# Optimization experiments

Measured on AMD Instinct MI355X. Metric: run time of the kernel, lower is better.

## Reference

```python
import jax, jax.numpy as jnp
import numpy as np

EPS = 1e-5

def _layernorm(x, gamma, beta):
    # normalize over last (channel) axis, per point
    mu = jnp.mean(x, axis=-1, keepdims=True)
    var = jnp.mean(jnp.square(x - mu), axis=-1, keepdims=True)
    return (x - mu) * jax.lax.rsqrt(var + EPS) * gamma + beta

def setup_inputs() -> dict:
    key = jax.random.key(0)
    ks = jax.random.split(key, 12)
    B, N, C, F = 32, 4096, 3, 1024
    points = jax.random.normal(ks[0], (B, N, C), dtype=jnp.float32)
    mask = jax.random.randint(ks[1], (B, 1, N), 0, 2, dtype=jnp.int32)
    s = 0.05
    return {
        "points": points,
        "mask": mask,
        "w1": jax.random.normal(ks[2], (128, C), dtype=jnp.float32) * s,      # conv1 (no bias)
        "g1": jnp.ones((128,), jnp.float32),                                   # norm1 gamma
        "be1": jnp.zeros((128,), jnp.float32),                                 # norm1 beta
        "w2": jax.random.normal(ks[3], (256, 128), dtype=jnp.float32) * s,     # conv2
        "b2": jax.random.normal(ks[4], (256,), dtype=jnp.float32) * s,
        "w3": jax.random.normal(ks[5], (512, 512), dtype=jnp.float32) * s,     # conv3 (no bias)
        "g2": jnp.ones((512,), jnp.float32),                                   # norm2 gamma
        "be2": jnp.zeros((512,), jnp.float32),                                 # norm2 beta
        "w4": jax.random.normal(ks[6], (F, 512), dtype=jnp.float32) * s,       # conv4
        "b4": jax.random.normal(ks[7], (F,), dtype=jnp.float32) * s,
    }

def reference(points, mask, w1, g1, be1, w2, b2, w3, g2, be2, w4, b4):
    # points: [B, N, C]; mask: [B, 1, N]
    vis = (mask[:, 0, :] != 0).astype(points.dtype)[..., None]  # [B, N, 1]
    # conv1 (1x1, no bias) as point-wise matmul
    h0 = jnp.einsum('bnc,kc->bnk', points, w1)                  # [B, N, 128]
    # masked LayerNorm: LN is per-point over channels, so compute densely and zero invisible points
    h1 = _layernorm(h0, g1, be1) * vis
    h2 = jax.nn.relu(h1)
    h3 = jnp.einsum('bnk,ok->bno', h2, w2) + b2                 # [B, N, 256]
    gmax = jnp.max(h3, axis=1, keepdims=True)                   # [B, 1, 256]
    dist = jnp.concatenate([jnp.broadcast_to(gmax, h3.shape), h3], axis=-1)  # [B, N, 512]
    h4 = jnp.einsum('bno,po->bnp', dist, w3)                    # [B, N, 512]
    h5 = _layernorm(h4, g2, be2) * vis
    h6 = jax.nn.relu(h5)
    h7 = jnp.einsum('bnp,fp->bnf', h6, w4) + b4                 # [B, N, F]
    return jnp.max(h7, axis=1)                                  # [B, F]
```

## Files before the change

### kernel.cpp

```cpp
#include <hip/hip_runtime.h>
#include <stdint.h>

#define LN_EPS 1e-5f

static __device__ __forceinline__ unsigned short f2bf_bits(float f) {
  union { float f; unsigned u; } v; v.f = f;
  unsigned r = v.u + 0x7FFFu + ((v.u >> 16) & 1u);
  return (unsigned short)(r >> 16);
}
static __device__ __forceinline__ float bf2f(unsigned short h) {
  union { unsigned u; float f; } v; v.u = ((unsigned)h) << 16;
  return v.f;
}

typedef __bf16 bf16x8 __attribute__((ext_vector_type(8)));
typedef float floatx4 __attribute__((ext_vector_type(4)));

typedef __attribute__((address_space(1))) unsigned int* gas_ptr;
typedef __attribute__((address_space(3))) unsigned int* las_ptr;
static __device__ __forceinline__ void async_cp16(const void* g, void* l) {
  __builtin_amdgcn_global_load_lds((gas_ptr)g, (las_ptr)l, 16, 0, 0);
}

__global__ __launch_bounds__(256) void perm_kernel(
    const int* __restrict__ mask, int* __restrict__ newrow, int* __restrict__ cnt) {
  const int b = blockIdx.x, t = threadIdx.x;
  const int base = b * 4096 + t * 16;
  int v[16]; int s = 0;
#pragma unroll
  for (int i = 0; i < 16; ++i) { v[i] = (mask[base + i] != 0); s += v[i]; }
  const int lane = t & 63, wv = t >> 6;
  int scan = s;
  for (int o = 1; o < 64; o <<= 1) { int x = __shfl_up(scan, o); if (lane >= o) scan += x; }
  __shared__ int wsum[4], woff[4], stotal;
  if (lane == 63) wsum[wv] = scan;
  __syncthreads();
  if (t == 0) { int a = 0; for (int k = 0; k < 4; ++k) { woff[k] = a; a += wsum[k]; } stotal = a; cnt[b] = a; }
  __syncthreads();
  const int excl = scan - s + woff[wv];
  const int total = stotal;
  int run = 0;
#pragma unroll
  for (int i = 0; i < 16; ++i) {
    const int pos = t * 16 + i;
    const int visBefore = excl + run;
    newrow[b * 4096 + pos] = v[i] ? visBefore : total + (pos - visBefore);
    run += v[i];
  }
}

__global__ __launch_bounds__(256) void conv1_ln_kernel(
    const float* __restrict__ points,
    const float* __restrict__ w1, const float* __restrict__ g1,
    const float* __restrict__ be1, unsigned short* __restrict__ h2,
    const int* __restrict__ newrow, const int* __restrict__ cnt,
    const float* __restrict__ w2, const float* __restrict__ b2,
    const float* __restrict__ w3, const float* __restrict__ w4,
    unsigned short* __restrict__ w2b, unsigned short* __restrict__ w4b,
    unsigned short* __restrict__ w23b, float* __restrict__ vecb) {
  if (blockIdx.x >= 32768) {
    const int bb = blockIdx.x - 32768;
    if (bb < 2176) {
      int idx = bb * 256 + threadIdx.x;
      if (idx < 32768) w2b[idx] = f2bf_bits(w2[idx]);
      else w4b[idx - 32768] = f2bf_bits(w4[idx - 32768]);
    } else {
      const int tid = threadIdx.x;
      const int p = (bb - 2176) * 2 + (tid >> 7);
      const int c = tid & 127;
      const float* w3r = w3 + (size_t)p * 512 + 256;
      float s = 0.f;
      for (int k = 0; k < 256; ++k) s += w3r[k] * w2[k * 128 + c];
      w23b[p * 128 + c] = f2bf_bits(s);
      if (c == 0) {
        float vb = 0.f;
        for (int k = 0; k < 256; ++k) vb += w3r[k] * b2[k];
        vecb[p] = vb;
      }
    }
    return;
  }
  const int lane = threadIdx.x & 63;
  const int wv = threadIdx.x >> 6;
  const size_t p = (size_t)blockIdx.x * 4 + wv;
  const int dest = newrow[p];
  const int cntb = cnt[p >> 12];
  const int ceilv = (cntb + 127) & ~127;
  if (dest >= ceilv) return;
  const bool vis = (dest < cntb);
  const float x0 = points[p * 3 + 0];
  const float x1 = points[p * 3 + 1];
  const float x2 = points[p * 3 + 2];
  const int c0 = lane * 2, c1 = c0 + 1;
  float h00 = w1[c0 * 3] * x0 + w1[c0 * 3 + 1] * x1 + w1[c0 * 3 + 2] * x2;
  float h01 = w1[c1 * 3] * x0 + w1[c1 * 3 + 1] * x1 + w1[c1 * 3 + 2] * x2;
  float s = h00 + h01;
  for (int o = 32; o; o >>= 1) s += __shfl_xor(s, o);
  const float mu = s * (1.f / 128.f);
  const float d0 = h00 - mu, d1 = h01 - mu;
  float q = d0 * d0 + d1 * d1;
  for (int o = 32; o; o >>= 1) q += __shfl_xor(q, o);
  const float rs = rsqrtf(q * (1.f / 128.f) + LN_EPS);
  const float y0 = vis ? fmaxf(d0 * rs * g1[c0] + be1[c0], 0.f) : 0.f;
  const float y1 = vis ? fmaxf(d1 * rs * g1[c1] + be1[c1], 0.f) : 0.f;
  union { unsigned u; unsigned short s2[2]; } pk;
  pk.s2[0] = f2bf_bits(y0);
  pk.s2[1] = f2bf_bits(y1);
  const size_t prow = (p & ~(size_t)4095) + (size_t)dest;
  ((unsigned*)h2)[prow * 64 + lane] = pk.u;
}

template <int EPI, int NCT>
__global__ __launch_bounds__(256) void gemm_bt(
    const unsigned short* __restrict__ A, const unsigned short* __restrict__ Bw,
    void* __restrict__ outp, float* __restrict__ outp2,
    const float* __restrict__ extra, const int* __restrict__ cnt,
    int M, int N, int K) {
  __shared__ __align__(16) char smA[2][128 * 64];
  __shared__ __align__(16) char smB[2][128 * 64];
  __shared__ float lmax[2][128];

  const int tid = threadIdx.x;
  const int lane = tid & 63;
  const int w = tid >> 6;
  const int wm = w >> 1, wn = w & 1;

  const int gid = blockIdx.x;
  const int xcd = gid & 7;
  const int slot = gid >> 3;
  const int rowsPerXcd = (M >> 7) >> 3;
  const int rowTile = xcd * rowsPerXcd + slot / NCT;
  const int colTile = slot % NCT;
  const size_t rowBase = (size_t)rowTile * 128;
  const int colBase = colTile * 128;

  const int cntb = cnt[rowBase >> 12];
  const int rb = (int)(rowBase & 4095);
  if (rb >= cntb) {
    if (EPI == 0) return;
    if (EPI == 2) {
      if (tid < 128) outp2[(size_t)rowTile * N + colBase + tid] = 0.f;
      return;
    }
    if (EPI == 4) {
      if (tid < 128) outp2[(size_t)rowTile * N + colBase + tid] = extra[colBase + tid];
      return;
    }
  }

  floatx4 acc[4][4];
  const floatx4 zero = {0.f, 0.f, 0.f, 0.f};
#pragma unroll
  for (int i = 0; i < 4; ++i)
#pragma unroll
    for (int j = 0; j < 4; ++j) acc[i][j] = zero;

  const int rSub = lane >> 2;
  const int cb16 = (lane & 3) * 16;
  const size_t Kb = (size_t)K * 2;
  const char* gA = (const char*)A + (rowBase + (size_t)(w * 32 + rSub)) * Kb + cb16;
  const char* gB = (const char*)Bw + ((size_t)colBase + (size_t)(w * 32 + rSub)) * Kb + cb16;
  char* lA0 = smA[0] + w * 2048;
  char* lA1 = smA[1] + w * 2048;
  char* lB0 = smB[0] + w * 2048;
  char* lB1 = smB[1] + w * 2048;
  const size_t skip16 = 16 * Kb;

  const int fm = lane & 15, fq = lane >> 4;
  const int fOff = fm * 64 + fq * 16;
  const char* pa0 = smA[0] + wm * 64 * 64 + fOff;
  const char* pa1 = smA[1] + wm * 64 * 64 + fOff;
  const char* pb0 = smB[0] + wn * 64 * 64 + fOff;
  const char* pb1 = smB[1] + wn * 64 * 64 + fOff;

  for (int k0 = 0; k0 < K; k0 += 64) {
    async_cp16(gA, lA0);
    async_cp16(gA + skip16, lA0 + 1024);
    async_cp16(gA + 64, lA1);
    async_cp16(gA + 64 + skip16, lA1 + 1024);
    async_cp16(gB, lB0);
    async_cp16(gB + skip16, lB0 + 1024);
    async_cp16(gB + 64, lB1);
    async_cp16(gB + 64 + skip16, lB1 + 1024);
    gA += 128; gB += 128;
    __syncthreads();
    bf16x8 af0[4], bg0[4], af1[4], bg1[4];
#pragma unroll
    for (int i = 0; i < 4; ++i) af0[i] = *(const bf16x8*)(pa0 + i * 16 * 64);
#pragma unroll
    for (int j = 0; j < 4; ++j) bg0[j] = *(const bf16x8*)(pb0 + j * 16 * 64);
#pragma unroll
    for (int i = 0; i < 4; ++i)
#pragma unroll
      for (int j = 0; j < 4; ++j)
        acc[i][j] = __builtin_amdgcn_mfma_f32_16x16x32_bf16(af0[i], bg0[j], acc[i][j], 0, 0, 0);
#pragma unroll
    for (int i = 0; i < 4; ++i) af1[i] = *(const bf16x8*)(pa1 + i * 16 * 64);
#pragma unroll
    for (int j = 0; j < 4; ++j) bg1[j] = *(const bf16x8*)(pb1 + j * 16 * 64);
#pragma unroll
    for (int i = 0; i < 4; ++i)
#pragma unroll
      for (int j = 0; j < 4; ++j)
        acc[i][j] = __builtin_amdgcn_mfma_f32_16x16x32_bf16(af1[i], bg1[j], acc[i][j], 0, 0, 0);
    __syncthreads();
  }

  float m4[4] = {-1e30f, -1e30f, -1e30f, -1e30f};

  if (EPI == 0) {
    unsigned short* O = (unsigned short*)outp;
#pragma unroll
    for (int j = 0; j < 4; ++j) {
      const int col = colBase + wn * 64 + j * 16 + fm;
      const float ex = extra[col];
#pragma unroll
      for (int i = 0; i < 4; ++i) {
        const size_t row0 = rowBase + wm * 64 + i * 16 + fq * 4;
#pragma unroll
        for (int r = 0; r < 4; ++r) {
          O[(row0 + r) * (size_t)N + col] = f2bf_bits(acc[i][j][r] + ex);
        }
      }
    }
  } else if (EPI == 2) {
#pragma unroll
    for (int j = 0; j < 4; ++j)
#pragma unroll
      for (int i = 0; i < 4; ++i)
#pragma unroll
        for (int r = 0; r < 4; ++r) m4[j] = fmaxf(m4[j], acc[i][j][r]);
  } else {
#pragma unroll
    for (int j = 0; j < 4; ++j) {
      const float ex = extra[colBase + wn * 64 + j * 16 + fm];
#pragma unroll
      for (int i = 0; i < 4; ++i)
#pragma unroll
        for (int r = 0; r < 4; ++r) m4[j] = fmaxf(m4[j], acc[i][j][r] + ex);
    }
  }

  if (EPI == 2 || EPI == 4) {
#pragma unroll
    for (int j = 0; j < 4; ++j) {
      m4[j] = fmaxf(m4[j], __shfl_xor(m4[j], 16));
      m4[j] = fmaxf(m4[j], __shfl_xor(m4[j], 32));
    }
    const float sel = (fq == 0) ? m4[0] : (fq == 1) ? m4[1] : (fq == 2) ? m4[2] : m4[3];
    lmax[wm][wn * 64 + fq * 16 + fm] = sel;
    __syncthreads();
    if (tid < 128) {
      const float v = fmaxf(lmax[0][tid], lmax[1][tid]);
      outp2[(size_t)rowTile * N + colBase + tid] = v;
    }
  }
}

__global__ __launch_bounds__(256) void gmax_cvec_kernel(
    const float* __restrict__ pg, const float* __restrict__ w3,
    float* __restrict__ cvec) {
  __shared__ float gm[256];
  const int b = blockIdx.x, t = threadIdx.x;
  float m = -1e30f;
  for (int s = 0; s < 32; ++s) m = fmaxf(m, pg[((size_t)b * 32 + s) * 256 + t]);
  gm[t] = m;
  __syncthreads();
#pragma unroll
  for (int half = 0; half < 2; ++half) {
    const int p = half * 256 + t;
    const float* wr = w3 + (size_t)p * 512;
    float s = 0.f;
    for (int c = 0; c < 256; ++c) s += wr[c] * gm[c];
    cvec[b * 512 + p] = s;
  }
}

__global__ __launch_bounds__(256) void ln2_kernel(
    unsigned short* __restrict__ h46, const int* __restrict__ cnt,
    const float* __restrict__ cvec,
    const float* __restrict__ g2, const float* __restrict__ be2) {
  const int lane = threadIdx.x & 63;
  const int wv = threadIdx.x >> 6;
  const size_t p = (size_t)blockIdx.x * 4 + wv;
  const int cb = cnt[p >> 12];
  const int pin = (int)(p & 4095);
  const int ceilv = (cb + 127) & ~127;
  if (pin >= ceilv) return;
  unsigned short* row = h46 + p * 512;
  const int c0 = lane * 8;
  if (pin >= cb) {
    const uint4 z = {0, 0, 0, 0};
    *(uint4*)(row + c0) = z;
    return;
  }
  const int b = (int)(p >> 12);
  union { uint4 v; unsigned short s[8]; } in;
  in.v = *(const uint4*)(row + c0);
  float cv[8];
  *(float4*)(cv) = *(const float4*)(cvec + b * 512 + c0);
  *(float4*)(cv + 4) = *(const float4*)(cvec + b * 512 + c0 + 4);
  float f[8];
  float s = 0.f;
#pragma unroll
  for (int k = 0; k < 8; ++k) { f[k] = bf2f(in.s[k]) + cv[k]; s += f[k]; }
  for (int o = 32; o; o >>= 1) s += __shfl_xor(s, o);
  const float mu = s * (1.f / 512.f);
  float q = 0.f;
#pragma unroll
  for (int k = 0; k < 8; ++k) { const float d = f[k] - mu; q += d * d; }
  for (int o = 32; o; o >>= 1) q += __shfl_xor(q, o);
  const float rs = rsqrtf(q * (1.f / 512.f) + LN_EPS);
  union { uint4 v; unsigned short s[8]; } outv;
#pragma unroll
  for (int k = 0; k < 8; ++k) {
    const float y = fmaxf((f[k] - mu) * rs * g2[c0 + k] + be2[c0 + k], 0.f);
    outv.s[k] = f2bf_bits(y);
  }
  *(uint4*)(row + c0) = outv.v;
}

__global__ __launch_bounds__(256) void final_kernel(
    const float* __restrict__ pmax, const float* __restrict__ b4,
    float* __restrict__ out) {
  const int idx = blockIdx.x * 256 + threadIdx.x;
  const int b = idx >> 10, f = idx & 1023;
  float m = -1e30f;
  for (int r = 0; r < 32; ++r) m = fmaxf(m, pmax[((size_t)(b * 32 + r)) * 1024 + f]);
  out[idx] = m + b4[f];
}

extern "C" void kernel_launch(void* const* d_in, const int* in_sizes, int n_in,
                              void* d_out, int out_size, void* d_ws, size_t ws_size,
                              hipStream_t stream) {
  const float* points = (const float*)d_in[0];
  const int* mask = (const int*)d_in[1];
  const float* w1 = (const float*)d_in[2];
  const float* g1 = (const float*)d_in[3];
  const float* be1 = (const float*)d_in[4];
  const float* w2 = (const float*)d_in[5];
  const float* b2 = (const float*)d_in[6];
  const float* w3 = (const float*)d_in[7];
  const float* g2 = (const float*)d_in[8];
  const float* be2 = (const float*)d_in[9];
  const float* w4 = (const float*)d_in[10];
  const float* b4 = (const float*)d_in[11];
  float* out = (float*)d_out;
  char* ws = (char*)d_ws;

  const size_t OFF_H46 = 0;
  const size_t OFF_H2 = 134217728;
  const size_t OFF_W2B = OFF_H2 + 33554432;
  const size_t OFF_W4B = OFF_W2B + 65536;
  const size_t OFF_W23B = OFF_W4B + 1048576;
  const size_t OFF_VECB = OFF_W23B + 131072;
  const size_t OFF_PG = OFF_VECB + 2048;
  const size_t OFF_CVEC = OFF_PG + 1048576;
  const size_t OFF_PMAX = OFF_CVEC + 65536;
  const size_t OFF_CNT = OFF_PMAX + 4194304;
  const size_t OFF_NEWROW = OFF_CNT + 4096;

  unsigned short* h2 = (unsigned short*)(ws + OFF_H2);
  unsigned short* h46 = (unsigned short*)(ws + OFF_H46);
  unsigned short* w2b = (unsigned short*)(ws + OFF_W2B);
  unsigned short* w4b = (unsigned short*)(ws + OFF_W4B);
  unsigned short* w23b = (unsigned short*)(ws + OFF_W23B);
  float* vecb = (float*)(ws + OFF_VECB);
  float* pg = (float*)(ws + OFF_PG);
  float* cvecp = (float*)(ws + OFF_CVEC);
  float* pmaxp = (float*)(ws + OFF_PMAX);
  int* cntp = (int*)(ws + OFF_CNT);
  int* newrow = (int*)(ws + OFF_NEWROW);

  perm_kernel<<<32, 256, 0, stream>>>(mask, newrow, cntp);
  conv1_ln_kernel<<<32768 + 2176 + 256, 256, 0, stream>>>(
      points, w1, g1, be1, h2, newrow, cntp, w2, b2, w3, w4, w2b, w4b, w23b, vecb);
  gemm_bt<4, 2><<<2048, 256, 0, stream>>>(h2, w2b, nullptr, pg, b2, cntp, 131072, 256, 128);
  gmax_cvec_kernel<<<32, 256, 0, stream>>>(pg, w3, cvecp);
  gemm_bt<0, 4><<<4096, 256, 0, stream>>>(h2, w23b, (void*)h46, nullptr, vecb, cntp, 131072, 512, 128);
  ln2_kernel<<<32768, 256, 0, stream>>>(h46, cntp, cvecp, g2, be2);
  gemm_bt<2, 8><<<8192, 256, 0, stream>>>(h46, w4b, nullptr, pmaxp, nullptr, cntp, 131072, 1024, 512);
  final_kernel<<<128, 256, 0, stream>>>(pmaxp, b4, out);
}
```

Before: 283.8 us.

## Fuse conv2 max-pool GEMM and conv3 local GEMM into one launch; parallelize cvec

Merges the two GEMMs that both read h2 (the conv2 row-max GEMM and the w23 local-term GEMM) into a single kernel with six column tiles per row tile. The first two tiles produce per-tile maxima and the rest write bf16 h46, so one launch replaces two and h2 tiles can be reused through cache. The gmax_cvec kernel is spread over 128 blocks using float4 loads and wave shuffles instead of 32 blocks of serial dot products. The old templated GEMM is specialised into a max-only variant for the final layer. Risks are divergent epilogues within one grid and extra register pressure.

```diff
diff --git a/kernel.cpp b/kernel.cpp
--- a/kernel.cpp
+++ b/kernel.cpp
@@ -110,11 +110,139 @@
   ((unsigned*)h2)[prow * 64 + lane] = pk.u;
 }
 
-template <int EPI, int NCT>
-__global__ __launch_bounds__(256) void gemm_bt(
+__global__ __launch_bounds__(256) void gemm23_fused(
+    const unsigned short* __restrict__ A,
+    const unsigned short* __restrict__ w2b, const unsigned short* __restrict__ w23b,
+    unsigned short* __restrict__ h46, float* __restrict__ pg,
+    const float* __restrict__ b2, const float* __restrict__ vecb,
+    const int* __restrict__ cnt, int M) {
+  __shared__ __align__(16) char smA[2][128 * 64];
+  __shared__ __align__(16) char smB[2][128 * 64];
+  __shared__ float lmax[2][128];
+
+  const int tid = threadIdx.x;
+  const int lane = tid & 63;
+  const int w = tid >> 6;
+  const int wm = w >> 1, wn = w & 1;
+
+  const int gid = blockIdx.x;
+  const int xcd = gid & 7;
+  const int slot = gid >> 3;
+  const int rowsPerXcd = (M >> 7) >> 3;
+  const int rowTile = xcd * rowsPerXcd + slot / 6;
+  const int colTile = slot % 6;
+  const bool isPG = (colTile < 2);
+  const int colBase = isPG ? colTile * 128 : (colTile - 2) * 128;
+  const size_t rowBase = (size_t)rowTile * 128;
+  const unsigned short* Bw = isPG ? w2b : w23b;
+
+  const int cntb = cnt[rowBase >> 12];
+  const int rb = (int)(rowBase & 4095);
+  if (rb >= cntb) {
+    if (isPG) {
+      if (tid < 128) pg[(size_t)rowTile * 256 + colBase + tid] = b2[colBase + tid];
+    }
+    return;
+  }
+
+  floatx4 acc[4][4];
+  const floatx4 zero = {0.f, 0.f, 0.f, 0.f};
+#pragma unroll
+  for (int i = 0; i < 4; ++i)
+#pragma unroll
+    for (int j = 0; j < 4; ++j) acc[i][j] = zero;
+
+  const int rSub = lane >> 2;
+  const int cb16 = (lane & 3) * 16;
+  const size_t Kb = 256;
+  const char* gA = (const char*)A + (rowBase + (size_t)(w * 32 + rSub)) * Kb + cb16;
+  const char* gB = (const char*)Bw + ((size_t)colBase + (size_t)(w * 32 + rSub)) * Kb + cb16;
+  char* lA0 = smA[0] + w * 2048;
+  char* lA1 = smA[1] + w * 2048;
+  char* lB0 = smB[0] + w * 2048;
+  char* lB1 = smB[1] + w * 2048;
+  const size_t skip16 = 16 * Kb;
+
+  const int fm = lane & 15, fq = lane >> 4;
+  const int fOff = fm * 64 + fq * 16;
+  const char* pa0 = smA[0] + wm * 64 * 64 + fOff;
+  const char* pa1 = smA[1] + wm * 64 * 64 + fOff;
+  const char* pb0 = smB[0] + wn * 64 * 64 + fOff;
+  const char* pb1 = smB[1] + wn * 64 * 64 + fOff;
+
+  for (int k0 = 0; k0 < 128; k0 += 64) {
+    async_cp16(gA, lA0);
+    async_cp16(gA + skip16, lA0 + 1024);
+    async_cp16(gA + 64, lA1);
+    async_cp16(gA + 64 + skip16, lA1 + 1024);
+    async_cp16(gB, lB0);
+    async_cp16(gB + skip16, lB0 + 1024);
+    async_cp16(gB + 64, lB1);
+    async_cp16(gB + 64 + skip16, lB1 + 1024);
+    gA += 128; gB += 128;
+    __syncthreads();
+    bf16x8 af0[4], bg0[4], af1[4], bg1[4];
+#pragma unroll
+    for (int i = 0; i < 4; ++i) af0[i] = *(const bf16x8*)(pa0 + i * 16 * 64);
+#pragma unroll
+    for (int j = 0; j < 4; ++j) bg0[j] = *(const bf16x8*)(pb0 + j * 16 * 64);
+#pragma unroll
+    for (int i = 0; i < 4; ++i)
+#pragma unroll
+      for (int j = 0; j < 4; ++j)
+        acc[i][j] = __builtin_amdgcn_mfma_f32_16x16x32_bf16(af0[i], bg0[j], acc[i][j], 0, 0, 0);
+#pragma unroll
+    for (int i = 0; i < 4; ++i) af1[i] = *(const bf16x8*)(pa1 + i * 16 * 64);
+#pragma unroll
+    for (int j = 0; j < 4; ++j) bg1[j] = *(const bf16x8*)(pb1 + j * 16 * 64);
+#pragma unroll
+    for (int i = 0; i < 4; ++i)
+#pragma unroll
+      for (int j = 0; j < 4; ++j)
+        acc[i][j] = __builtin_amdgcn_mfma_f32_16x16x32_bf16(af1[i], bg1[j], acc[i][j], 0, 0, 0);
+    __syncthreads();
+  }
+
+  if (isPG) {
+    float m4[4] = {-1e30f, -1e30f, -1e30f, -1e30f};
+#pragma unroll
+    for (int j = 0; j < 4; ++j) {
+      const float ex = b2[colBase + wn * 64 + j * 16 + fm];
+#pragma unroll
+      for (int i = 0; i < 4; ++i)
+#pragma unroll
+        for (int r = 0; r < 4; ++r) m4[j] = fmaxf(m4[j], acc[i][j][r] + ex);
+      m4[j] = fmaxf(m4[j], __shfl_xor(m4[j], 16));
+      m4[j] = fmaxf(m4[j], __shfl_xor(m4[j], 32));
+    }
+    const float sel = (fq == 0) ? m4[0] : (fq == 1) ? m4[1] : (fq == 2) ? m4[2] : m4[3];
+    lmax[wm][wn * 64 + fq * 16 + fm] = sel;
+    __syncthreads();
+    if (tid < 128) {
+      const float v = fmaxf(lmax[0][tid], lmax[1][tid]);
+      pg[(size_t)rowTile * 256 + colBase + tid] = v;
+    }
+  } else {
+#pragma unroll
+    for (int j = 0; j < 4; ++j) {
+      const int col = colBase + wn * 64 + j * 16 + fm;
+      const float ex = vecb[col];
+#pragma unroll
+      for (int i = 0; i < 4; ++i) {
+        const size_t row0 = rowBase + wm * 64 + i * 16 + fq * 4;
+#pragma unroll
+        for (int r = 0; r < 4; ++r) {
+          h46[(row0 + r) * 512 + col] = f2bf_bits(acc[i][j][r] + ex);
+        }
+      }
+    }
+  }
+}
+
+template <int NCT>
+__global__ __launch_bounds__(256) void gemm4_kernel(
     const unsigned short* __restrict__ A, const unsigned short* __restrict__ Bw,
-    void* __restrict__ outp, float* __restrict__ outp2,
-    const float* __restrict__ extra, const int* __restrict__ cnt,
+    float* __restrict__ outp2, const int* __restrict__ cnt,
     int M, int N, int K) {
   __shared__ __align__(16) char smA[2][128 * 64];
   __shared__ __align__(16) char smB[2][128 * 64];
@@ -137,15 +265,8 @@
   const int cntb = cnt[rowBase >> 12];
   const int rb = (int)(rowBase & 4095);
   if (rb >= cntb) {
-    if (EPI == 0) return;
-    if (EPI == 2) {
-      if (tid < 128) outp2[(size_t)rowTile * N + colBase + tid] = 0.f;
-      return;
-    }
-    if (EPI == 4) {
-      if (tid < 128) outp2[(size_t)rowTile * N + colBase + tid] = extra[colBase + tid];
-      return;
-    }
+    if (tid < 128) outp2[(size_t)rowTile * N + colBase + tid] = 0.f;
+    return;
   }
 
   floatx4 acc[4][4];
@@ -207,53 +328,21 @@
   }
 
   float m4[4] = {-1e30f, -1e30f, -1e30f, -1e30f};
-
-  if (EPI == 0) {
-    unsigned short* O = (unsigned short*)outp;
-#pragma unroll
-    for (int j = 0; j < 4; ++j) {
-      const int col = colBase + wn * 64 + j * 16 + fm;
-      const float ex = extra[col];
-#pragma unroll
-      for (int i = 0; i < 4; ++i) {
-        const size_t row0 = rowBase + wm * 64 + i * 16 + fq * 4;
-#pragma unroll
-        for (int r = 0; r < 4; ++r) {
-          O[(row0 + r) * (size_t)N + col] = f2bf_bits(acc[i][j][r] + ex);
-        }
-      }
-    }
-  } else if (EPI == 2) {
-#pragma unroll
-    for (int j = 0; j < 4; ++j)
-#pragma unroll
-      for (int i = 0; i < 4; ++i)
-#pragma unroll
-        for (int r = 0; r < 4; ++r) m4[j] = fmaxf(m4[j], acc[i][j][r]);
-  } else {
-#pragma unroll
-    for (int j = 0; j < 4; ++j) {
-      const float ex = extra[colBase + wn * 64 + j * 16 + fm];
-#pragma unroll
-      for (int i = 0; i < 4; ++i)
-#pragma unroll
-        for (int r = 0; r < 4; ++r) m4[j] = fmaxf(m4[j], acc[i][j][r] + ex);
-    }
-  }
-
-  if (EPI == 2 || EPI == 4) {
-#pragma unroll
-    for (int j = 0; j < 4; ++j) {
-      m4[j] = fmaxf(m4[j], __shfl_xor(m4[j], 16));
-      m4[j] = fmaxf(m4[j], __shfl_xor(m4[j], 32));
-    }
-    const float sel = (fq == 0) ? m4[0] : (fq == 1) ? m4[1] : (fq == 2) ? m4[2] : m4[3];
-    lmax[wm][wn * 64 + fq * 16 + fm] = sel;
-    __syncthreads();
-    if (tid < 128) {
-      const float v = fmaxf(lmax[0][tid], lmax[1][tid]);
-      outp2[(size_t)rowTile * N + colBase + tid] = v;
-    }
+#pragma unroll
+  for (int j = 0; j < 4; ++j) {
+#pragma unroll
+    for (int i = 0; i < 4; ++i)
+#pragma unroll
+      for (int r = 0; r < 4; ++r) m4[j] = fmaxf(m4[j], acc[i][j][r]);
+    m4[j] = fmaxf(m4[j], __shfl_xor(m4[j], 16));
+    m4[j] = fmaxf(m4[j], __shfl_xor(m4[j], 32));
+  }
+  const float sel = (fq == 0) ? m4[0] : (fq == 1) ? m4[1] : (fq == 2) ? m4[2] : m4[3];
+  lmax[wm][wn * 64 + fq * 16 + fm] = sel;
+  __syncthreads();
+  if (tid < 128) {
+    const float v = fmaxf(lmax[0][tid], lmax[1][tid]);
+    outp2[(size_t)rowTile * N + colBase + tid] = v;
   }
 }
 
@@ -261,18 +350,23 @@
     const float* __restrict__ pg, const float* __restrict__ w3,
     float* __restrict__ cvec) {
   __shared__ float gm[256];
-  const int b = blockIdx.x, t = threadIdx.x;
+  const int b = blockIdx.x >> 2, quarter = blockIdx.x & 3;
+  const int t = threadIdx.x;
   float m = -1e30f;
   for (int s = 0; s < 32; ++s) m = fmaxf(m, pg[((size_t)b * 32 + s) * 256 + t]);
   gm[t] = m;
   __syncthreads();
-#pragma unroll
-  for (int half = 0; half < 2; ++half) {
-    const int p = half * 256 + t;
-    const float* wr = w3 + (size_t)p * 512;
-    float s = 0.f;
-    for (int c = 0; c < 256; ++c) s += wr[c] * gm[c];
-    cvec[b * 512 + p] = s;
+  const int lane = t & 63, wv = t >> 6;
+  const float g0 = gm[lane * 4 + 0];
+  const float g1 = gm[lane * 4 + 1];
+  const float g2v = gm[lane * 4 + 2];
+  const float g3 = gm[lane * 4 + 3];
+  for (int pp = 0; pp < 32; ++pp) {
+    const int p = quarter * 128 + wv * 32 + pp;
+    const float4 wr = *(const float4*)(w3 + (size_t)p * 512 + lane * 4);
+    float s = wr.x * g0 + wr.y * g1 + wr.z * g2v + wr.w * g3;
+    for (int o = 32; o; o >>= 1) s += __shfl_xor(s, o);
+    if (lane == 0) cvec[b * 512 + p] = s;
   }
 }
 
@@ -375,10 +469,9 @@
   perm_kernel<<<32, 256, 0, stream>>>(mask, newrow, cntp);
   conv1_ln_kernel<<<32768 + 2176 + 256, 256, 0, stream>>>(
       points, w1, g1, be1, h2, newrow, cntp, w2, b2, w3, w4, w2b, w4b, w23b, vecb);
-  gemm_bt<4, 2><<<2048, 256, 0, stream>>>(h2, w2b, nullptr, pg, b2, cntp, 131072, 256, 128);
-  gmax_cvec_kernel<<<32, 256, 0, stream>>>(pg, w3, cvecp);
-  gemm_bt<0, 4><<<4096, 256, 0, stream>>>(h2, w23b, (void*)h46, nullptr, vecb, cntp, 131072, 512, 128);
+  gemm23_fused<<<6144, 256, 0, stream>>>(h2, w2b, w23b, h46, pg, b2, vecb, cntp, 131072);
+  gmax_cvec_kernel<<<128, 256, 0, stream>>>(pg, w3, cvecp);
   ln2_kernel<<<32768, 256, 0, stream>>>(h46, cntp, cvecp, g2, be2);
-  gemm_bt<2, 8><<<8192, 256, 0, stream>>>(h46, w4b, nullptr, pmaxp, nullptr, cntp, 131072, 1024, 512);
+  gemm4_kernel<8><<<8192, 256, 0, stream>>>(h46, w4b, pmaxp, cntp, 131072, 1024, 512);
   final_kernel<<<128, 256, 0, stream>>>(pmaxp, b4, out);
 }
```

New measurement: 276.6 us (median of 2 runs). 1.03x faster.
